# Kernel optimization log

Hardware: AMD Instinct MI355X
Metric: run time of the kernel (lower is better)

## Reference

```python
import jax, jax.numpy as jnp
import numpy as np

B, C, W, H = 4, 128, 64, 64

def setup_inputs() -> dict:
    key = jax.random.key(0)
    ks = jax.random.split(key, 10)
    s = 1.0 / np.sqrt(C)
    return {
        "x": jax.random.normal(ks[0], (B, C, W, H), dtype=jnp.float32),
        "wq": jax.random.normal(ks[1], (C, C), dtype=jnp.float32) * s,
        "bq": jax.random.normal(ks[2], (C,), dtype=jnp.float32) * s,
        "wk": jax.random.normal(ks[3], (C, C), dtype=jnp.float32) * s,
        "bk": jax.random.normal(ks[4], (C,), dtype=jnp.float32) * s,
        "wv": jax.random.normal(ks[5], (C, C), dtype=jnp.float32) * s,
        "bv": jax.random.normal(ks[6], (C,), dtype=jnp.float32) * s,
        "wo": jax.random.normal(ks[7], (C, C), dtype=jnp.float32) * s,
        "bo": jax.random.normal(ks[8], (C,), dtype=jnp.float32) * s,
        "gamma": jax.random.normal(ks[9], (1,), dtype=jnp.float32),
    }

def reference(x, wq, bq, wk, bk, wv, bv, wo, bo, gamma):
    b, c, w, h = x.shape
    n = w * h
    xf = x.reshape(b, c, n)  # [B,C,N]
    # 1x1 conv == per-position matmul over channels
    q = jnp.einsum('oc,bcn->bon', wq, xf) + bq[:, None]
    k = jnp.einsum('oc,bcn->bon', wk, xf) + bk[:, None]
    v = jnp.einsum('oc,bcn->bon', wv, xf) + bv[:, None]
    # attention[b,n,m] = sum_c q[b,c,n] * k[b,c,m]
    scores = jnp.einsum('bcn,bcm->bnm', q, k) / jnp.sqrt(jnp.asarray(c, x.dtype))
    attn = jax.nn.softmax(scores, axis=-1)  # [B,N,N]
    # out[b,c,n] = sum_m v[b,c,m] * attn[b,n,m]
    out = jnp.einsum('bcm,bnm->bcn', v, attn)
    y = jnp.einsum('oc,bcn->bon', wo, out) + bo[:, None]
    y = y.reshape(b, c, w, h)
    return gamma[0] * y + x
```

## Files before the change

### kernel.cpp

```cpp
#include <hip/hip_runtime.h>

#define BN 4
#define CH 128
#define NN 4096
#define SCALE_QL2 0.12751744954339238f

typedef __attribute__((ext_vector_type(8))) short s8b;
typedef __attribute__((ext_vector_type(4))) float f32x4;
typedef __attribute__((ext_vector_type(8))) unsigned short us8;
typedef __attribute__((ext_vector_type(4))) unsigned short us4;

#define MFMA16(a, b, c) __builtin_amdgcn_mfma_f32_16x16x32_bf16((a), (b), (c), 0, 0, 0)

#define GLOAD16(gsrc, ldst) __builtin_amdgcn_global_load_lds( \
    (const __attribute__((address_space(1))) unsigned int*)(gsrc), \
    (__attribute__((address_space(3))) unsigned int*)(ldst), 16, 0, 0)

__device__ __forceinline__ unsigned short f2bf(float f) {
  union { float f; unsigned int u; } v; v.f = f;
  unsigned int r = v.u + 0x7fffu + ((v.u >> 16) & 1u);
  return (unsigned short)(r >> 16);
}
__device__ __forceinline__ float bf2f(unsigned short h) {
  union { unsigned int u; float f; } v; v.u = (unsigned int)h << 16;
  return v.f;
}

__global__ __launch_bounds__(256, 2) void qkv_fused(
    const float* __restrict__ x,
    const float* __restrict__ wq, const float* __restrict__ bq,
    const float* __restrict__ wk, const float* __restrict__ bk,
    const float* __restrict__ wv, const float* __restrict__ bv,
    unsigned short* __restrict__ Qt, unsigned short* __restrict__ Kt,
    unsigned short* __restrict__ Vn)
{
  __shared__ __align__(16) unsigned short Xh[64 * 128];
  __shared__ __align__(16) unsigned short Xl[64 * 128];

  const int b = blockIdx.y;
  const int n0 = blockIdx.x * 64;
  const int z = blockIdx.z;
  const float* W; const float* bias;
  if (z == 0)      { W = wq; bias = bq; }
  else if (z == 1) { W = wk; bias = bk; }
  else             { W = wv; bias = bv; }
  const float* Xb = x + (size_t)b * CH * NN;

  const int tid = threadIdx.x;
  const int w = tid >> 6, lane = tid & 63, l15 = lane & 15, g = lane >> 4;
  const int ob = w * 32;

#pragma unroll
  for (int it = 0; it < 8; ++it) {
    int idx = it * 256 + tid;
    int c = idx >> 4;
    int n4 = (idx & 15) * 4;
    float4 v = *reinterpret_cast<const float4*>(&Xb[(size_t)c * NN + n0 + n4]);
    float vv[4] = {v.x, v.y, v.z, v.w};
#pragma unroll
    for (int k = 0; k < 4; ++k) {
      int n = n4 + k;
      unsigned short hh = f2bf(vv[k]);
      unsigned short ll = f2bf(vv[k] - bf2f(hh));
      int ad = n * 128 + (c ^ ((n & 7) << 3));
      Xh[ad] = hh;
      Xl[ad] = ll;
    }
  }

  s8b ah[2][4], al[2][4];
#pragma unroll
  for (int m = 0; m < 2; ++m)
#pragma unroll
    for (int kk = 0; kk < 4; ++kk) {
      int o = ob + m * 16 + l15;
      int c = (kk * 4 + g) * 8;
      float4 w0 = *reinterpret_cast<const float4*>(&W[o * CH + c]);
      float4 w1 = *reinterpret_cast<const float4*>(&W[o * CH + c + 4]);
      float wv8[8] = {w0.x, w0.y, w0.z, w0.w, w1.x, w1.y, w1.z, w1.w};
      s8b hh, ll;
#pragma unroll
      for (int t = 0; t < 8; ++t) {
        unsigned short hv = f2bf(wv8[t]);
        hh[t] = (short)hv;
        ll[t] = (short)f2bf(wv8[t] - bf2f(hv));
      }
      ah[m][kk] = hh;
      al[m][kk] = ll;
    }
  __syncthreads();

  f32x4 acc[2][4];
#pragma unroll
  for (int m = 0; m < 2; ++m)
#pragma unroll
    for (int nst = 0; nst < 4; ++nst)
#pragma unroll
      for (int r = 0; r < 4; ++r) acc[m][nst][r] = 0.f;

#pragma unroll
  for (int kk = 0; kk < 4; ++kk)
#pragma unroll
    for (int nst = 0; nst < 4; ++nst) {
      int n = nst * 16 + l15;
      int ck = (kk * 4 + g) ^ (n & 7);
      s8b bh = *reinterpret_cast<const s8b*>(&Xh[n * 128 + ck * 8]);
      s8b bl = *reinterpret_cast<const s8b*>(&Xl[n * 128 + ck * 8]);
#pragma unroll
      for (int m = 0; m < 2; ++m) {
        acc[m][nst] = MFMA16(ah[m][kk], bh, acc[m][nst]);
        acc[m][nst] = MFMA16(ah[m][kk], bl, acc[m][nst]);
        acc[m][nst] = MFMA16(al[m][kk], bh, acc[m][nst]);
      }
    }
  __syncthreads();

  if (z < 2) {
    const float s = (z == 0) ? SCALE_QL2 : 1.f;
#pragma unroll
    for (int m = 0; m < 2; ++m) {
      float4 b4 = *reinterpret_cast<const float4*>(&bias[ob + m * 16 + g * 4]);
      float bb[4] = {b4.x, b4.y, b4.z, b4.w};
#pragma unroll
      for (int nst = 0; nst < 4; ++nst) {
        int n = nst * 16 + l15;
        int slot = w * 8 + m * 4 + g;
        int sl = slot ^ (n & 7);
        us4 pk;
#pragma unroll
        for (int r = 0; r < 4; ++r) pk[r] = f2bf((acc[m][nst][r] + bb[r]) * s);
        *reinterpret_cast<us4*>(&Xh[n * 128 + sl * 4]) = pk;
      }
    }
    __syncthreads();
    unsigned short* T = (z == 0 ? Qt : Kt) + ((size_t)b * NN + n0) * CH;
#pragma unroll
    for (int it = 0; it < 4; ++it) {
      int idx = it * 256 + tid;
      int n = idx >> 4;
      int j = idx & 15;
      int s0 = (2 * j) ^ (n & 7);
      int s1 = (2 * j + 1) ^ (n & 7);
      us4 a4 = *reinterpret_cast<const us4*>(&Xh[n * 128 + s0 * 4]);
      us4 b4 = *reinterpret_cast<const us4*>(&Xh[n * 128 + s1 * 4]);
      us8 o8;
#pragma unroll
      for (int t = 0; t < 4; ++t) { o8[t] = a4[t]; o8[4 + t] = b4[t]; }
      *reinterpret_cast<us8*>(&T[n * CH + j * 8]) = o8;
    }
  } else {
#pragma unroll
    for (int m = 0; m < 2; ++m) {
      float4 b4 = *reinterpret_cast<const float4*>(&bias[ob + m * 16 + g * 4]);
      float bb[4] = {b4.x, b4.y, b4.z, b4.w};
#pragma unroll
      for (int nst = 0; nst < 4; ++nst) {
        int n = nst * 16 + l15;
#pragma unroll
        for (int r = 0; r < 4; ++r) {
          int o = ob + m * 16 + g * 4 + r;
          Xh[o * 64 + (n ^ ((o & 7) << 3))] = f2bf(acc[m][nst][r] + bb[r]);
        }
      }
    }
    __syncthreads();
    unsigned short* V = Vn + (size_t)b * CH * NN;
#pragma unroll
    for (int it = 0; it < 4; ++it) {
      int idx = it * 256 + tid;
      int o = idx >> 3;
      int j8 = idx & 7;
      us8 v8 = *reinterpret_cast<const us8*>(&Xh[o * 64 + ((j8 ^ (o & 7)) << 3)]);
      *reinterpret_cast<us8*>(&V[(size_t)o * NN + n0 + j8 * 8]) = v8;
    }
  }
}

__global__ __launch_bounds__(256, 2) void flash_attn_v4(
    const unsigned short* __restrict__ Qt,
    const unsigned short* __restrict__ Kt,
    const unsigned short* __restrict__ Vn,
    unsigned short* __restrict__ Oth, unsigned short* __restrict__ Otl)
{
  __shared__ __align__(16) unsigned char smem[73728];

  const int flat = blockIdx.y * 128 + blockIdx.x;
  const int swz = (flat & 7) * 64 + (flat >> 3);
  const int b = swz >> 7;
  const int n0 = (swz & 127) * 32;

  const int tid = threadIdx.x;
  const int w = tid >> 6, lane = tid & 63, l15 = lane & 15, g = lane >> 4;

  const unsigned short* Qb = Qt + (size_t)b * NN * CH;
  const unsigned short* Kb = Kt + (size_t)b * NN * CH;
  const unsigned short* Vb = Vn + (size_t)b * CH * NN;

  s8b qf[2][4];
#pragma unroll
  for (int m = 0; m < 2; ++m)
#pragma unroll
    for (int kk = 0; kk < 4; ++kk) {
      int row = n0 + m * 16 + l15;
      int c = (kk * 4 + g) * 8;
      qf[m][kk] = *reinterpret_cast<const s8b*>(&Qb[(size_t)row * CH + c]);
    }

  f32x4 facc[2][8];
#pragma unroll
  for (int m = 0; m < 2; ++m)
#pragma unroll
    for (int cst = 0; cst < 8; ++cst)
#pragma unroll
      for (int r = 0; r < 4; ++r) facc[m][cst][r] = 0.f;
  float m_run[2][4], l_run[2][4];
#pragma unroll
  for (int m = 0; m < 2; ++m)
#pragma unroll
    for (int r = 0; r < 4; ++r) { m_run[m][r] = -1e30f; l_run[m][r] = 0.f; }

  const unsigned short* Ks = (const unsigned short*)smem;
  const unsigned short* Vs = (const unsigned short*)(smem + 32768);
  unsigned short* Pw = (unsigned short*)(smem + 65536) + w * 1024;

  for (int kt = 0; kt < 32; ++kt) {
    const int m0 = kt * 128;
    __syncthreads();
#pragma unroll
    for (int i = 0; i < 8; ++i) {
      int loff = i * 4096 + tid * 16;
      int row = loff >> 8;
      int chunk = (loff >> 4) & 15;
      int sk = chunk ^ (row & 7);
      GLOAD16(Kb + (size_t)(m0 + row) * CH + sk * 8, smem + loff);
      GLOAD16(Vb + (size_t)row * NN + m0 + sk * 8, smem + 32768 + loff);
    }
    __syncthreads();

    f32x4 sacc[2][2];
#pragma unroll
    for (int m = 0; m < 2; ++m)
#pragma unroll
      for (int st = 0; st < 2; ++st)
#pragma unroll
        for (int r = 0; r < 4; ++r) sacc[m][st][r] = 0.f;
    __builtin_amdgcn_s_setprio(1);
#pragma unroll
    for (int kk = 0; kk < 4; ++kk)
#pragma unroll
      for (int st = 0; st < 2; ++st) {
        int key = w * 32 + st * 16 + l15;
        int ck = (kk * 4 + g) ^ (key & 7);
        s8b bf = *reinterpret_cast<const s8b*>(&Ks[key * 128 + ck * 8]);
        sacc[0][st] = MFMA16(qf[0][kk], bf, sacc[0][st]);
        sacc[1][st] = MFMA16(qf[1][kk], bf, sacc[1][st]);
      }
    __builtin_amdgcn_s_setprio(0);

#pragma unroll
    for (int m = 0; m < 2; ++m)
#pragma unroll
      for (int r = 0; r < 4; ++r) {
        float s0 = sacc[m][0][r], s1 = sacc[m][1][r];
        float mt = fmaxf(s0, s1);
        mt = fmaxf(mt, __shfl_xor(mt, 1));
        mt = fmaxf(mt, __shfl_xor(mt, 2));
        mt = fmaxf(mt, __shfl_xor(mt, 4));
        mt = fmaxf(mt, __shfl_xor(mt, 8));
        if (__any(mt > m_run[m][r] + 8.f)) {
          float mn = fmaxf(m_run[m][r], mt);
          float f = exp2f(m_run[m][r] - mn);
          l_run[m][r] *= f;
#pragma unroll
          for (int cst = 0; cst < 8; ++cst) facc[m][cst][r] *= f;
          m_run[m][r] = mn;
        }
        float p0 = exp2f(s0 - m_run[m][r]);
        float p1 = exp2f(s1 - m_run[m][r]);
        l_run[m][r] += p0 + p1;
        int rw = m * 16 + g * 4 + r;
        int sch0 = (l15 >> 3) ^ g;
        int sch1 = (2 + (l15 >> 3)) ^ g;
        Pw[rw * 32 + sch0 * 8 + (l15 & 7)] = f2bf(p0);
        Pw[rw * 32 + sch1 * 8 + (l15 & 7)] = f2bf(p1);
      }

    s8b pa[2];
#pragma unroll
    for (int m = 0; m < 2; ++m) {
      int row = m * 16 + l15;
      int sch = g ^ (l15 >> 2);
      pa[m] = *reinterpret_cast<const s8b*>(&Pw[row * 32 + sch * 8]);
    }
    __builtin_amdgcn_s_setprio(1);
#pragma unroll
    for (int cst = 0; cst < 8; ++cst) {
      int c = cst * 16 + l15;
      int ck = (w * 4 + g) ^ (c & 7);
      s8b vf = *reinterpret_cast<const s8b*>(&Vs[c * 128 + ck * 8]);
      facc[0][cst] = MFMA16(pa[0], vf, facc[0][cst]);
      facc[1][cst] = MFMA16(pa[1], vf, facc[1][cst]);
    }
    __builtin_amdgcn_s_setprio(0);
  }

  float l_red[2][4];
#pragma unroll
  for (int m = 0; m < 2; ++m)
#pragma unroll
    for (int r = 0; r < 4; ++r) {
      float rs = l_run[m][r];
      rs += __shfl_xor(rs, 1);
      rs += __shfl_xor(rs, 2);
      rs += __shfl_xor(rs, 4);
      rs += __shfl_xor(rs, 8);
      l_red[m][r] = rs;
    }
  __syncthreads();

  float* Mb = (float*)smem;
  float* Lb = (float*)(smem + 512);
  float* Db = (float*)(smem + 1024);
  float* Obuf = (float*)(smem + 2048);

  if (l15 == 0) {
#pragma unroll
    for (int m = 0; m < 2; ++m)
#pragma unroll
      for (int r = 0; r < 4; ++r) {
        int ra = m * 16 + g * 4 + r;
        Mb[w * 32 + ra] = m_run[m][r];
        Lb[w * 32 + ra] = l_red[m][r];
      }
  }
  __syncthreads();
  float fsc[2][4];
#pragma unroll
  for (int m = 0; m < 2; ++m)
#pragma unroll
    for (int r = 0; r < 4; ++r) {
      int ra = m * 16 + g * 4 + r;
      float M = fmaxf(fmaxf(Mb[ra], Mb[32 + ra]), fmaxf(Mb[64 + ra], Mb[96 + ra]));
      fsc[m][r] = exp2f(m_run[m][r] - M);
      if (w == 0 && l15 == 0) {
        float den = Lb[ra] * exp2f(Mb[ra] - M) + Lb[32 + ra] * exp2f(Mb[32 + ra] - M) +
                    Lb[64 + ra] * exp2f(Mb[64 + ra] - M) +
                    Lb[96 + ra] * exp2f(Mb[96 + ra] - M);
        Db[ra] = 1.f / den;
      }
    }
#pragma unroll
  for (int t = 0; t < 4; ++t) {
    __syncthreads();
    if (w == t) {
#pragma unroll
      for (int m = 0; m < 2; ++m)
#pragma unroll
        for (int cst = 0; cst < 8; ++cst)
#pragma unroll
          for (int r = 0; r < 4; ++r) {
            int ra = m * 16 + g * 4 + r;
            int c = cst * 16 + l15;
            float v = facc[m][cst][r] * fsc[m][r];
            if (t == 0) Obuf[ra * 132 + c] = v;
            else        Obuf[ra * 132 + c] += v;
          }
    }
  }
  __syncthreads();
#pragma unroll
  for (int it = 0; it < 2; ++it) {
    int idx = it * 256 + tid;
    int row = idx >> 4;
    int j = idx & 15;
    float inv = Db[row];
    float4 v0 = *reinterpret_cast<const float4*>(&Obuf[row * 132 + j * 8]);
    float4 v1 = *reinterpret_cast<const float4*>(&Obuf[row * 132 + j * 8 + 4]);
    float vv[8] = {v0.x, v0.y, v0.z, v0.w, v1.x, v1.y, v1.z, v1.w};
    us8 hh, ll;
#pragma unroll
    for (int t = 0; t < 8; ++t) {
      float v = vv[t] * inv;
      unsigned short hv = f2bf(v);
      hh[t] = hv;
      ll[t] = f2bf(v - bf2f(hv));
    }
    size_t go = ((size_t)b * NN + n0 + row) * CH + j * 8;
    *reinterpret_cast<us8*>(&Oth[go]) = hh;
    *reinterpret_cast<us8*>(&Otl[go]) = ll;
  }
}

__global__ __launch_bounds__(256, 2) void out_mfma(
    const unsigned short* __restrict__ Oth, const unsigned short* __restrict__ Otl,
    const float* __restrict__ wo, const float* __restrict__ bo,
    const float* __restrict__ x, const float* __restrict__ gamma,
    float* __restrict__ y)
{
  __shared__ __align__(16) unsigned char smem[67584];
  unsigned short* Oh = (unsigned short*)smem;
  unsigned short* Ol = (unsigned short*)(smem + 16384);
  float* Obuf = (float*)(smem + 32768);

  const int b = blockIdx.y;
  const int n0 = blockIdx.x * 64;
  const int tid = threadIdx.x;
  const int w = tid >> 6, lane = tid & 63, l15 = lane & 15, g = lane >> 4;
  const int ob = w * 32;

  const unsigned short* OhB = Oth + ((size_t)b * NN + n0) * CH;
  const unsigned short* OlB = Otl + ((size_t)b * NN + n0) * CH;
#pragma unroll
  for (int i = 0; i < 4; ++i) {
    int base = i * 4096 + w * 1024;
    int loff = base + lane * 16;
    int row = loff >> 8;
    int chunk = (loff >> 4) & 15;
    int sk = chunk ^ (row & 7);
    GLOAD16(OhB + (size_t)row * CH + sk * 8, smem + base);
    GLOAD16(OlB + (size_t)row * CH + sk * 8, smem + 16384 + base);
  }

  s8b ah[2][4], al[2][4];
#pragma unroll
  for (int m = 0; m < 2; ++m)
#pragma unroll
    for (int kk = 0; kk < 4; ++kk) {
      int o = ob + m * 16 + l15;
      int c = (kk * 4 + g) * 8;
      float4 w0 = *reinterpret_cast<const float4*>(&wo[o * CH + c]);
      float4 w1 = *reinterpret_cast<const float4*>(&wo[o * CH + c + 4]);
      float wv8[8] = {w0.x, w0.y, w0.z, w0.w, w1.x, w1.y, w1.z, w1.w};
      s8b hh, ll;
#pragma unroll
      for (int t = 0; t < 8; ++t) {
        unsigned short hv = f2bf(wv8[t]);
        hh[t] = (short)hv;
        ll[t] = (short)f2bf(wv8[t] - bf2f(hv));
      }
      ah[m][kk] = hh;
      al[m][kk] = ll;
    }
  const float gm = gamma[0];
  __syncthreads();

  f32x4 acc[2][4];
#pragma unroll
  for (int m = 0; m < 2; ++m)
#pragma unroll
    for (int nst = 0; nst < 4; ++nst)
#pragma unroll
      for (int r = 0; r < 4; ++r) acc[m][nst][r] = 0.f;

#pragma unroll
  for (int kk = 0; kk < 4; ++kk)
#pragma unroll
    for (int nst = 0; nst < 4; ++nst) {
      int n = nst * 16 + l15;
      int ck = (kk * 4 + g) ^ (n & 7);
      s8b bh = *reinterpret_cast<const s8b*>(&Oh[n * 128 + ck * 8]);
      s8b bl = *reinterpret_cast<const s8b*>(&Ol[n * 128 + ck * 8]);
#pragma unroll
      for (int m = 0; m < 2; ++m) {
        acc[m][nst] = MFMA16(ah[m][kk], bh, acc[m][nst]);
        acc[m][nst] = MFMA16(ah[m][kk], bl, acc[m][nst]);
        acc[m][nst] = MFMA16(al[m][kk], bh, acc[m][nst]);
      }
    }
  __syncthreads();

#pragma unroll
  for (int m = 0; m < 2; ++m) {
    float4 b4 = *reinterpret_cast<const float4*>(&bo[ob + m * 16 + g * 4]);
    float bb[4] = {b4.x, b4.y, b4.z, b4.w};
#pragma unroll
    for (int nst = 0; nst < 4; ++nst) {
      int n = nst * 16 + l15;
#pragma unroll
      for (int r = 0; r < 4; ++r) {
        int o = ob + m * 16 + g * 4 + r;
        Obuf[o * 68 + n] = gm * (acc[m][nst][r] + bb[r]);
      }
    }
  }
  __syncthreads();
  const float* Xb = x + (size_t)b * CH * NN;
  float* Yb = y + (size_t)b * CH * NN;
#pragma unroll
  for (int it = 0; it < 8; ++it) {
    int idx = it * 256 + tid;
    int o = idx >> 4;
    int n4 = (idx & 15) * 4;
    float4 v = *reinterpret_cast<const float4*>(&Obuf[o * 68 + n4]);
    float4 rx = *reinterpret_cast<const float4*>(&Xb[(size_t)o * NN + n0 + n4]);
    v.x += rx.x; v.y += rx.y; v.z += rx.z; v.w += rx.w;
    *reinterpret_cast<float4*>(&Yb[(size_t)o * NN + n0 + n4]) = v;
  }
}

extern "C" void kernel_launch(void* const* d_in, const int* in_sizes, int n_in,
                              void* d_out, int out_size, void* d_ws, size_t ws_size,
                              hipStream_t stream) {
  const float* x     = (const float*)d_in[0];
  const float* wq    = (const float*)d_in[1];
  const float* bq    = (const float*)d_in[2];
  const float* wk    = (const float*)d_in[3];
  const float* bk    = (const float*)d_in[4];
  const float* wv    = (const float*)d_in[5];
  const float* bv    = (const float*)d_in[6];
  const float* wo    = (const float*)d_in[7];
  const float* bo    = (const float*)d_in[8];
  const float* gamma = (const float*)d_in[9];
  float* y = (float*)d_out;

  const size_t per = (size_t)BN * NN * CH;
  unsigned short* Qt  = (unsigned short*)d_ws;
  unsigned short* Kt  = Qt + per;
  unsigned short* Vn  = Kt + per;
  unsigned short* Oth = Vn + per;
  unsigned short* Otl = Oth + per;

  qkv_fused<<<dim3(NN / 64, BN, 3), 256, 0, stream>>>(x, wq, bq, wk, bk, wv, bv,
                                                      Qt, Kt, Vn);
  flash_attn_v4<<<dim3(NN / 32, BN), 256, 0, stream>>>(Qt, Kt, Vn, Oth, Otl);
  out_mfma<<<dim3(NN / 64, BN), 256, 0, stream>>>(Oth, Otl, wo, bo, x, gamma, y);
}
```

Baseline: 204.3 us.

## Load K and V fragments directly from global memory instead of staging in LDS

```diff
diff --git a/kernel.cpp b/kernel.cpp
--- a/kernel.cpp
+++ b/kernel.cpp
@@ -176,13 +176,13 @@
   }
 }
 
-__global__ __launch_bounds__(256, 2) void flash_attn_v4(
+__global__ __launch_bounds__(256, 3) void flash_attn_v5(
     const unsigned short* __restrict__ Qt,
     const unsigned short* __restrict__ Kt,
     const unsigned short* __restrict__ Vn,
     unsigned short* __restrict__ Oth, unsigned short* __restrict__ Otl)
 {
-  __shared__ __align__(16) unsigned char smem[73728];
+  __shared__ __align__(16) unsigned char smem[18944];
 
   const int flat = blockIdx.y * 128 + blockIdx.x;
   const int swz = (flat & 7) * 64 + (flat >> 3);
@@ -219,23 +219,17 @@
 #pragma unroll
     for (int r = 0; r < 4; ++r) { m_run[m][r] = -1e30f; l_run[m][r] = 0.f; }
 
-  const unsigned short* Ks = (const unsigned short*)smem;
-  const unsigned short* Vs = (const unsigned short*)(smem + 32768);
-  unsigned short* Pw = (unsigned short*)(smem + 65536) + w * 1024;
-
-  for (int kt = 0; kt < 32; ++kt) {
-    const int m0 = kt * 128;
-    __syncthreads();
-#pragma unroll
-    for (int i = 0; i < 8; ++i) {
-      int loff = i * 4096 + tid * 16;
-      int row = loff >> 8;
-      int chunk = (loff >> 4) & 15;
-      int sk = chunk ^ (row & 7);
-      GLOAD16(Kb + (size_t)(m0 + row) * CH + sk * 8, smem + loff);
-      GLOAD16(Vb + (size_t)row * NN + m0 + sk * 8, smem + 32768 + loff);
-    }
-    __syncthreads();
+  for (int t = 0; t < 32; ++t) {
+    const int key0 = (t * 4 + w) * 32;
+    unsigned short* Pt = (unsigned short*)smem + w * 2048 + (t & 1) * 1024;
+
+    s8b kf[2][4];
+#pragma unroll
+    for (int st = 0; st < 2; ++st)
+#pragma unroll
+      for (int kk = 0; kk < 4; ++kk)
+        kf[st][kk] = *reinterpret_cast<const s8b*>(
+            &Kb[(size_t)(key0 + st * 16 + l15) * CH + (kk * 4 + g) * 8]);
 
     f32x4 sacc[2][2];
 #pragma unroll
@@ -249,11 +243,8 @@
     for (int kk = 0; kk < 4; ++kk)
 #pragma unroll
       for (int st = 0; st < 2; ++st) {
-        int key = w * 32 + st * 16 + l15;
-        int ck = (kk * 4 + g) ^ (key & 7);
-        s8b bf = *reinterpret_cast<const s8b*>(&Ks[key * 128 + ck * 8]);
-        sacc[0][st] = MFMA16(qf[0][kk], bf, sacc[0][st]);
-        sacc[1][st] = MFMA16(qf[1][kk], bf, sacc[1][st]);
+        sacc[0][st] = MFMA16(qf[0][kk], kf[st][kk], sacc[0][st]);
+        sacc[1][st] = MFMA16(qf[1][kk], kf[st][kk], sacc[1][st]);
       }
     __builtin_amdgcn_s_setprio(0);
 
@@ -281,8 +272,8 @@
         int rw = m * 16 + g * 4 + r;
         int sch0 = (l15 >> 3) ^ g;
         int sch1 = (2 + (l15 >> 3)) ^ g;
-        Pw[rw * 32 + sch0 * 8 + (l15 & 7)] = f2bf(p0);
-        Pw[rw * 32 + sch1 * 8 + (l15 & 7)] = f2bf(p1);
+        Pt[rw * 32 + sch0 * 8 + (l15 & 7)] = f2bf(p0);
+        Pt[rw * 32 + sch1 * 8 + (l15 & 7)] = f2bf(p1);
       }
 
     s8b pa[2];
@@ -290,14 +281,13 @@
     for (int m = 0; m < 2; ++m) {
       int row = m * 16 + l15;
       int sch = g ^ (l15 >> 2);
-      pa[m] = *reinterpret_cast<const s8b*>(&Pw[row * 32 + sch * 8]);
+      pa[m] = *reinterpret_cast<const s8b*>(&Pt[row * 32 + sch * 8]);
     }
     __builtin_amdgcn_s_setprio(1);
 #pragma unroll
     for (int cst = 0; cst < 8; ++cst) {
       int c = cst * 16 + l15;
-      int ck = (w * 4 + g) ^ (c & 7);
-      s8b vf = *reinterpret_cast<const s8b*>(&Vs[c * 128 + ck * 8]);
+      s8b vf = *reinterpret_cast<const s8b*>(&Vb[(size_t)c * NN + key0 + g * 8]);
       facc[0][cst] = MFMA16(pa[0], vf, facc[0][cst]);
       facc[1][cst] = MFMA16(pa[1], vf, facc[1][cst]);
     }
@@ -522,6 +512,6 @@
 
   qkv_fused<<<dim3(NN / 64, BN, 3), 256, 0, stream>>>(x, wq, bq, wk, bk, wv, bv,
                                                       Qt, Kt, Vn);
-  flash_attn_v4<<<dim3(NN / 32, BN), 256, 0, stream>>>(Qt, Kt, Vn, Oth, Otl);
+  flash_attn_v5<<<dim3(NN / 32, BN), 256, 0, stream>>>(Qt, Kt, Vn, Oth, Otl);
   out_mfma<<<dim3(NN / 64, BN), 256, 0, stream>>>(Oth, Otl, wo, bo, x, gamma, y);
 }
```

After: 258.1 us. 1.26x slower.

## Restructure flash attention to 64-query blocks with 8 waves and transposed MFMA

Applied to the files above, without the earlier changes.

```diff
diff --git a/kernel.cpp b/kernel.cpp
--- a/kernel.cpp
+++ b/kernel.cpp
@@ -9,6 +9,7 @@
 typedef __attribute__((ext_vector_type(4))) float f32x4;
 typedef __attribute__((ext_vector_type(8))) unsigned short us8;
 typedef __attribute__((ext_vector_type(4))) unsigned short us4;
+typedef __attribute__((ext_vector_type(2))) unsigned int u32x2;
 
 #define MFMA16(a, b, c) __builtin_amdgcn_mfma_f32_16x16x32_bf16((a), (b), (c), 0, 0, 0)
 
@@ -24,6 +25,16 @@
 __device__ __forceinline__ float bf2f(unsigned short h) {
   union { unsigned int u; float f; } v; v.u = (unsigned int)h << 16;
   return v.f;
+}
+__device__ __forceinline__ float fexp2(float x) {
+  float r;
+  asm("v_exp_f32 %0, %1" : "=v"(r) : "v"(x));
+  return r;
+}
+__device__ __forceinline__ unsigned int pk2(float a, float b) {
+  unsigned int r;
+  asm("v_cvt_pk_bf16_f32 %0, %1, %2" : "=v"(r) : "v"(a), "v"(b));
+  return r;
 }
 
 __global__ __launch_bounds__(256, 2) void qkv_fused(
@@ -176,201 +187,201 @@
   }
 }
 
-__global__ __launch_bounds__(256, 2) void flash_attn_v4(
+__global__ __launch_bounds__(512, 2) void flash_attn_v6(
     const unsigned short* __restrict__ Qt,
     const unsigned short* __restrict__ Kt,
     const unsigned short* __restrict__ Vn,
     unsigned short* __restrict__ Oth, unsigned short* __restrict__ Otl)
 {
-  __shared__ __align__(16) unsigned char smem[73728];
-
-  const int flat = blockIdx.y * 128 + blockIdx.x;
-  const int swz = (flat & 7) * 64 + (flat >> 3);
-  const int b = swz >> 7;
-  const int n0 = (swz & 127) * 32;
+  __shared__ __align__(16) unsigned char smem[81920];
+
+  const int flat = blockIdx.y * 64 + blockIdx.x;
+  const int swz = (flat & 7) * 32 + (flat >> 3);
+  const int b = swz >> 6;
+  const int n0 = (swz & 63) * 64;
 
   const int tid = threadIdx.x;
   const int w = tid >> 6, lane = tid & 63, l15 = lane & 15, g = lane >> 4;
+  const int rhalf = w & 1;
+  const int h = w >> 1;
 
   const unsigned short* Qb = Qt + (size_t)b * NN * CH;
   const unsigned short* Kb = Kt + (size_t)b * NN * CH;
   const unsigned short* Vb = Vn + (size_t)b * CH * NN;
 
-  s8b qf[2][4];
-#pragma unroll
-  for (int m = 0; m < 2; ++m)
-#pragma unroll
-    for (int kk = 0; kk < 4; ++kk) {
-      int row = n0 + m * 16 + l15;
-      int c = (kk * 4 + g) * 8;
-      qf[m][kk] = *reinterpret_cast<const s8b*>(&Qb[(size_t)row * CH + c]);
-    }
-
-  f32x4 facc[2][8];
-#pragma unroll
-  for (int m = 0; m < 2; ++m)
-#pragma unroll
-    for (int cst = 0; cst < 8; ++cst)
-#pragma unroll
-      for (int r = 0; r < 4; ++r) facc[m][cst][r] = 0.f;
-  float m_run[2][4], l_run[2][4];
-#pragma unroll
-  for (int m = 0; m < 2; ++m)
-#pragma unroll
-    for (int r = 0; r < 4; ++r) { m_run[m][r] = -1e30f; l_run[m][r] = 0.f; }
-
   const unsigned short* Ks = (const unsigned short*)smem;
   const unsigned short* Vs = (const unsigned short*)(smem + 32768);
   unsigned short* Pw = (unsigned short*)(smem + 65536) + w * 1024;
 
+  s8b qf[2][4];
+#pragma unroll
+  for (int qh = 0; qh < 2; ++qh)
+#pragma unroll
+    for (int kk = 0; kk < 4; ++kk) {
+      int row = n0 + rhalf * 32 + qh * 16 + l15;
+      int c = (kk * 4 + g) * 8;
+      qf[qh][kk] = *reinterpret_cast<const s8b*>(&Qb[(size_t)row * CH + c]);
+    }
+
+  f32x4 facc[2][8];
+#pragma unroll
+  for (int qh = 0; qh < 2; ++qh)
+#pragma unroll
+    for (int cst = 0; cst < 8; ++cst)
+#pragma unroll
+      for (int r = 0; r < 4; ++r) facc[qh][cst][r] = 0.f;
+  float m_run[2] = {-1e30f, -1e30f};
+  float l_run[2] = {0.f, 0.f};
+
+  const int x2 = (l15 & 3) << 1;
+  const int ppx = g ^ (l15 & 3);
+
   for (int kt = 0; kt < 32; ++kt) {
     const int m0 = kt * 128;
     __syncthreads();
 #pragma unroll
-    for (int i = 0; i < 8; ++i) {
-      int loff = i * 4096 + tid * 16;
+    for (int i = 0; i < 4; ++i) {
+      int base = i * 8192 + w * 1024;
+      int loff = base + lane * 16;
       int row = loff >> 8;
       int chunk = (loff >> 4) & 15;
       int sk = chunk ^ (row & 7);
-      GLOAD16(Kb + (size_t)(m0 + row) * CH + sk * 8, smem + loff);
-      GLOAD16(Vb + (size_t)row * NN + m0 + sk * 8, smem + 32768 + loff);
+      GLOAD16(Kb + (size_t)(m0 + row) * CH + sk * 8, smem + base);
+      GLOAD16(Vb + (size_t)row * NN + m0 + sk * 8, smem + 32768 + base);
     }
     __syncthreads();
 
     f32x4 sacc[2][2];
 #pragma unroll
-    for (int m = 0; m < 2; ++m)
+    for (int qh = 0; qh < 2; ++qh)
 #pragma unroll
       for (int st = 0; st < 2; ++st)
 #pragma unroll
-        for (int r = 0; r < 4; ++r) sacc[m][st][r] = 0.f;
+        for (int r = 0; r < 4; ++r) sacc[qh][st][r] = 0.f;
     __builtin_amdgcn_s_setprio(1);
 #pragma unroll
     for (int kk = 0; kk < 4; ++kk)
 #pragma unroll
       for (int st = 0; st < 2; ++st) {
-        int key = w * 32 + st * 16 + l15;
+        int key = h * 32 + st * 16 + l15;
         int ck = (kk * 4 + g) ^ (key & 7);
-        s8b bf = *reinterpret_cast<const s8b*>(&Ks[key * 128 + ck * 8]);
-        sacc[0][st] = MFMA16(qf[0][kk], bf, sacc[0][st]);
-        sacc[1][st] = MFMA16(qf[1][kk], bf, sacc[1][st]);
+        s8b kf = *reinterpret_cast<const s8b*>(&Ks[key * 128 + ck * 8]);
+        sacc[0][st] = MFMA16(kf, qf[0][kk], sacc[0][st]);
+        sacc[1][st] = MFMA16(kf, qf[1][kk], sacc[1][st]);
       }
     __builtin_amdgcn_s_setprio(0);
 
 #pragma unroll
-    for (int m = 0; m < 2; ++m)
-#pragma unroll
-      for (int r = 0; r < 4; ++r) {
-        float s0 = sacc[m][0][r], s1 = sacc[m][1][r];
-        float mt = fmaxf(s0, s1);
-        mt = fmaxf(mt, __shfl_xor(mt, 1));
-        mt = fmaxf(mt, __shfl_xor(mt, 2));
-        mt = fmaxf(mt, __shfl_xor(mt, 4));
-        mt = fmaxf(mt, __shfl_xor(mt, 8));
-        if (__any(mt > m_run[m][r] + 8.f)) {
-          float mn = fmaxf(m_run[m][r], mt);
-          float f = exp2f(m_run[m][r] - mn);
-          l_run[m][r] *= f;
-#pragma unroll
-          for (int cst = 0; cst < 8; ++cst) facc[m][cst][r] *= f;
-          m_run[m][r] = mn;
+    for (int qh = 0; qh < 2; ++qh) {
+      float s0 = sacc[qh][0][0], s1 = sacc[qh][0][1];
+      float s2 = sacc[qh][0][2], s3 = sacc[qh][0][3];
+      float s4 = sacc[qh][1][0], s5 = sacc[qh][1][1];
+      float s6 = sacc[qh][1][2], s7 = sacc[qh][1][3];
+      float m8 = fmaxf(fmaxf(fmaxf(s0, s1), fmaxf(s2, s3)),
+                       fmaxf(fmaxf(s4, s5), fmaxf(s6, s7)));
+      float mt = fmaxf(m8, __shfl_xor(m8, 16));
+      mt = fmaxf(mt, __shfl_xor(mt, 32));
+      if (__any(mt > m_run[qh] + 8.f)) {
+        float mn = fmaxf(m_run[qh], mt);
+        float f = fexp2(m_run[qh] - mn);
+        l_run[qh] *= f;
+#pragma unroll
+        for (int cst = 0; cst < 8; ++cst) {
+          facc[qh][cst][0] *= f; facc[qh][cst][1] *= f;
+          facc[qh][cst][2] *= f; facc[qh][cst][3] *= f;
         }
-        float p0 = exp2f(s0 - m_run[m][r]);
-        float p1 = exp2f(s1 - m_run[m][r]);
-        l_run[m][r] += p0 + p1;
-        int rw = m * 16 + g * 4 + r;
-        int sch0 = (l15 >> 3) ^ g;
-        int sch1 = (2 + (l15 >> 3)) ^ g;
-        Pw[rw * 32 + sch0 * 8 + (l15 & 7)] = f2bf(p0);
-        Pw[rw * 32 + sch1 * 8 + (l15 & 7)] = f2bf(p1);
-      }
+        m_run[qh] = mn;
+      }
+      float mr = m_run[qh];
+      float e0 = fexp2(s0 - mr), e1 = fexp2(s1 - mr);
+      float e2 = fexp2(s2 - mr), e3 = fexp2(s3 - mr);
+      float e4 = fexp2(s4 - mr), e5 = fexp2(s5 - mr);
+      float e6 = fexp2(s6 - mr), e7 = fexp2(s7 - mr);
+      l_run[qh] += ((e0 + e1) + (e2 + e3)) + ((e4 + e5) + (e6 + e7));
+      u32x2 w0, w1;
+      w0[0] = pk2(e0, e1); w0[1] = pk2(e2, e3);
+      w1[0] = pk2(e4, e5); w1[1] = pk2(e6, e7);
+      unsigned short* pb = Pw + qh * 512 + l15 * 32;
+      *reinterpret_cast<u32x2*>(pb + ((g ^ x2) << 2)) = w0;
+      *reinterpret_cast<u32x2*>(pb + (((4 + g) ^ x2) << 2)) = w1;
+    }
 
     s8b pa[2];
 #pragma unroll
-    for (int m = 0; m < 2; ++m) {
-      int row = m * 16 + l15;
-      int sch = g ^ (l15 >> 2);
-      pa[m] = *reinterpret_cast<const s8b*>(&Pw[row * 32 + sch * 8]);
-    }
+    for (int qh = 0; qh < 2; ++qh)
+      pa[qh] = *reinterpret_cast<const s8b*>(Pw + qh * 512 + l15 * 32 + ppx * 8);
     __builtin_amdgcn_s_setprio(1);
 #pragma unroll
     for (int cst = 0; cst < 8; ++cst) {
       int c = cst * 16 + l15;
-      int ck = (w * 4 + g) ^ (c & 7);
+      int ck = (h * 4 + g) ^ (c & 7);
       s8b vf = *reinterpret_cast<const s8b*>(&Vs[c * 128 + ck * 8]);
-      facc[0][cst] = MFMA16(pa[0], vf, facc[0][cst]);
-      facc[1][cst] = MFMA16(pa[1], vf, facc[1][cst]);
+      facc[0][cst] = MFMA16(vf, pa[0], facc[0][cst]);
+      facc[1][cst] = MFMA16(vf, pa[1], facc[1][cst]);
     }
     __builtin_amdgcn_s_setprio(0);
   }
 
-  float l_red[2][4];
-#pragma unroll
-  for (int m = 0; m < 2; ++m)
-#pragma unroll
-    for (int r = 0; r < 4; ++r) {
-      float rs = l_run[m][r];
-      rs += __shfl_xor(rs, 1);
-      rs += __shfl_xor(rs, 2);
-      rs += __shfl_xor(rs, 4);
-      rs += __shfl_xor(rs, 8);
-      l_red[m][r] = rs;
-    }
+  float l_red[2];
+#pragma unroll
+  for (int qh = 0; qh < 2; ++qh) {
+    float rs = l_run[qh];
+    rs += __shfl_xor(rs, 16);
+    rs += __shfl_xor(rs, 32);
+    l_red[qh] = rs;
+  }
   __syncthreads();
 
   float* Mb = (float*)smem;
-  float* Lb = (float*)(smem + 512);
-  float* Db = (float*)(smem + 1024);
-  float* Obuf = (float*)(smem + 2048);
-
-  if (l15 == 0) {
-#pragma unroll
-    for (int m = 0; m < 2; ++m)
-#pragma unroll
-      for (int r = 0; r < 4; ++r) {
-        int ra = m * 16 + g * 4 + r;
-        Mb[w * 32 + ra] = m_run[m][r];
-        Lb[w * 32 + ra] = l_red[m][r];
-      }
-  }
-  __syncthreads();
-  float fsc[2][4];
-#pragma unroll
-  for (int m = 0; m < 2; ++m)
-#pragma unroll
-    for (int r = 0; r < 4; ++r) {
-      int ra = m * 16 + g * 4 + r;
-      float M = fmaxf(fmaxf(Mb[ra], Mb[32 + ra]), fmaxf(Mb[64 + ra], Mb[96 + ra]));
-      fsc[m][r] = exp2f(m_run[m][r] - M);
-      if (w == 0 && l15 == 0) {
-        float den = Lb[ra] * exp2f(Mb[ra] - M) + Lb[32 + ra] * exp2f(Mb[32 + ra] - M) +
-                    Lb[64 + ra] * exp2f(Mb[64 + ra] - M) +
-                    Lb[96 + ra] * exp2f(Mb[96 + ra] - M);
-        Db[ra] = 1.f / den;
-      }
-    }
+  float* Lb = (float*)(smem + 1024);
+  float* Db = (float*)(smem + 2048);
+  float* Obuf = (float*)(smem + 4096);
+
+  if (g == 0) {
+#pragma unroll
+    for (int qh = 0; qh < 2; ++qh) {
+      int ra = rhalf * 32 + qh * 16 + l15;
+      Mb[h * 64 + ra] = m_run[qh];
+      Lb[h * 64 + ra] = l_red[qh];
+    }
+  }
+  __syncthreads();
+  float fsc[2];
+#pragma unroll
+  for (int qh = 0; qh < 2; ++qh) {
+    int ra = rhalf * 32 + qh * 16 + l15;
+    float M = fmaxf(fmaxf(Mb[ra], Mb[64 + ra]), fmaxf(Mb[128 + ra], Mb[192 + ra]));
+    fsc[qh] = fexp2(m_run[qh] - M);
+    if (h == 0 && g == 0) {
+      float den = Lb[ra] * fexp2(Mb[ra] - M) + Lb[64 + ra] * fexp2(Mb[64 + ra] - M) +
+                  Lb[128 + ra] * fexp2(Mb[128 + ra] - M) +
+                  Lb[192 + ra] * fexp2(Mb[192 + ra] - M);
+      Db[ra] = 1.f / den;
+    }
+  }
 #pragma unroll
   for (int t = 0; t < 4; ++t) {
     __syncthreads();
-    if (w == t) {
-#pragma unroll
-      for (int m = 0; m < 2; ++m)
+    if (h == t) {
+#pragma unroll
+      for (int qh = 0; qh < 2; ++qh) {
+        int ra = rhalf * 32 + qh * 16 + l15;
 #pragma unroll
         for (int cst = 0; cst < 8; ++cst)
 #pragma unroll
           for (int r = 0; r < 4; ++r) {
-            int ra = m * 16 + g * 4 + r;
-            int c = cst * 16 + l15;
-            float v = facc[m][cst][r] * fsc[m][r];
+            int c = cst * 16 + g * 4 + r;
+            float v = facc[qh][cst][r] * fsc[qh];
             if (t == 0) Obuf[ra * 132 + c] = v;
             else        Obuf[ra * 132 + c] += v;
           }
+      }
     }
   }
   __syncthreads();
 #pragma unroll
   for (int it = 0; it < 2; ++it) {
-    int idx = it * 256 + tid;
+    int idx = it * 512 + tid;
     int row = idx >> 4;
     int j = idx & 15;
     float inv = Db[row];
@@ -522,6 +533,6 @@
 
   qkv_fused<<<dim3(NN / 64, BN, 3), 256, 0, stream>>>(x, wq, bq, wk, bk, wv, bv,
                                                       Qt, Kt, Vn);
-  flash_attn_v4<<<dim3(NN / 32, BN), 256, 0, stream>>>(Qt, Kt, Vn, Oth, Otl);
+  flash_attn_v6<<<dim3(64, BN), 512, 0, stream>>>(Qt, Kt, Vn, Oth, Otl);
   out_mfma<<<dim3(NN / 64, BN), 256, 0, stream>>>(Oth, Otl, wo, bo, x, gamma, y);
 }
```

Result: faster. 168.1 us (-17.7%).
